# Kernel tuning notes

Measured on AMD Instinct MI355X. Metric: run time of the kernel, lower is better.

The kernel has to match this reference:

```python
import jax, jax.numpy as jnp
import numpy as np

NUM_CENTROIDS = 64
NUM_KMEANS = 5
KM_ITERS = 20


def _kmeans_labels(X, key):
    """Lloyd k-means on X [N,D]; returns final cluster labels [N] (int32).
    Mirrors faiss.Kmeans(dim, num_centroids, niter=...) label assignment."""
    N, D = X.shape
    idx = jax.random.choice(key, N, (NUM_CENTROIDS,), replace=False)
    cent0 = X[idx]  # [C,D] init from random data points

    def assign(cent):
        d = (cent * cent).sum(-1)[None, :] - 2.0 * (X @ cent.T)  # [N,C]
        return jnp.argmin(d, axis=1)

    def step(cent, _):
        lab = assign(cent)
        sums = jax.ops.segment_sum(X, lab, num_segments=NUM_CENTROIDS)  # [C,D]
        cnts = jax.ops.segment_sum(jnp.ones((N,), X.dtype), lab, num_segments=NUM_CENTROIDS)
        newc = jnp.where(cnts[:, None] > 0, sums / jnp.maximum(cnts, 1.0)[:, None], cent)
        return newc, None

    cent, _ = jax.lax.scan(step, cent0, None, length=KM_ITERS)
    return assign(cent)


def setup_inputs() -> dict:
    key = jax.random.key(0)
    k1, k2, k3 = jax.random.split(key, 3)
    N, D = 8192, 512
    adj = jax.random.uniform(k1, (N, N), dtype=jnp.float32)
    student = jax.random.normal(k2, (N, D), dtype=jnp.float32)
    teacher = jax.random.normal(k3, (N, D), dtype=jnp.float32)
    return {"adj": adj, "student": student, "teacher": teacher, "topk": 16}


def reference(adj, student, teacher, topk):
    N, D = student.shape
    # similarity = (student @ teacher.T).detach() + 10*I
    sim = jax.lax.stop_gradient(student @ teacher.T) + 10.0 * jnp.eye(N, dtype=student.dtype)
    _, I_knn = jax.lax.top_k(sim, topk)  # [N, k], sorted descending
    rows = jnp.arange(N)[:, None]  # [N,1]

    # knn_neighbor: sparse ones at (row, I_knn); topk cols are distinct per row
    knn_pat = jnp.zeros((N, N), adj.dtype).at[rows, I_knn].set(1.0)
    locality = knn_pat * adj  # sparse elementwise product knn_neighbor * adj

    # k-means cluster labels over NUM_KMEANS seeds (teacher is detached/cpu in torch)
    Xt = jax.lax.stop_gradient(teacher)
    keys = jax.random.split(jax.random.key(1234), NUM_KMEANS)
    labels = jax.vmap(lambda k: _kmeans_labels(Xt, k))(keys)  # [M,N]

    # close-in-background mask: any seed where label(i) == label(knn_j(i))
    ngh_lab = labels[:, I_knn]               # [M,N,k]
    mask = jnp.any(labels[:, :, None] == ngh_lab, axis=0)  # [N,k]

    # globality: ones at masked (row, knn) positions
    glob_pat = jnp.zeros((N, N), adj.dtype).at[rows, I_knn].add(mask.astype(adj.dtype))

    # pos = locality + globality (dense equivalent of coalesced sparse sum)
    pos = locality + glob_pat
    return pos
```

## Files before the change

kernel.cpp:

```cpp
#include <hip/hip_runtime.h>
#include <stdint.h>

typedef unsigned int u32;
typedef unsigned long long u64;
typedef __attribute__((ext_vector_type(8))) short short8;
typedef __attribute__((ext_vector_type(4))) float f32x4;

#define NN 8192
#define DD 512
#define CC 64
#define RR 5
#define KM_ITERS 20
#define TOPKK 16
#define CHUNK 4096
#define GAP_TH 0.05f
#define FLAGTH 0.02f
#define BAND_TH 0.01f
#define FIXCAP (RR * NN)
#define TK_LO 256.0f
#define TK_SCALE 8.0f

#define MFMA_BF16 __builtin_amdgcn_mfma_f32_16x16x32_bf16

__device__ __forceinline__ void gload16(void* lds, const void* g) {
  __builtin_amdgcn_global_load_lds(
      (const __attribute__((address_space(1))) void*)g,
      (__attribute__((address_space(3))) void*)lds, 16, 0, 0);
}

__device__ __forceinline__ u32 keyenc(float v) {
  u32 u = __float_as_uint(v);
  return (u & 0x80000000u) ? ~u : (u | 0x80000000u);
}
__device__ __forceinline__ int tkbin(float v) {
  int b = (int)((v + TK_LO) * TK_SCALE);
  return b < 0 ? 0 : (b > 4095 ? 4095 : b);
}

__device__ __forceinline__ void tf2x32(u32 k0, u32 k1, u32 x0, u32 x1,
                                       u32& o0, u32& o1) {
  u32 ks2 = k0 ^ k1 ^ 0x1BD11BDAu;
  x0 += k0; x1 += k1;
#define TFR(r) { x0 += x1; x1 = (x1 << r) | (x1 >> (32 - r)); x1 ^= x0; }
  TFR(13) TFR(15) TFR(26) TFR(6)
  x0 += k1; x1 += ks2 + 1u;
  TFR(17) TFR(29) TFR(16) TFR(24)
  x0 += ks2; x1 += k0 + 2u;
  TFR(13) TFR(15) TFR(26) TFR(6)
  x0 += k0; x1 += k1 + 3u;
  TFR(17) TFR(29) TFR(16) TFR(24)
  x0 += k1; x1 += ks2 + 4u;
  TFR(13) TFR(15) TFR(26) TFR(6)
  x0 += ks2; x1 += k0 + 5u;
#undef TFR
  o0 = x0; o1 = x1;
}

__global__ __launch_bounds__(256) void rng_kernel(u32* __restrict__ bits1,
                                                  u32* __restrict__ bits2) {
  int r = blockIdx.x;
  int i = blockIdx.y * 256 + threadIdx.x;
  u32 rk0, rk1; tf2x32(0u, 1234u, 0u, (u32)r, rk0, rk1);
  u32 k10, k11, s10, s11, s20, s21;
  tf2x32(rk0, rk1, 0u, 0u, k10, k11);
  tf2x32(rk0, rk1, 0u, 1u, s10, s11);
  tf2x32(k10, k11, 0u, 1u, s20, s21);
  u32 a, b;
  tf2x32(s10, s11, 0u, (u32)i, a, b);
  bits1[r * NN + i] = a ^ b;
  tf2x32(s20, s21, 0u, (u32)i, a, b);
  bits2[r * NN + i] = a ^ b;
}

__global__ __launch_bounds__(256) void rankpart_kernel(const u32* __restrict__ bits,
                                                       u32* __restrict__ prank) {
  __shared__ u64 sk[2048];
  int r = blockIdx.x, zc = blockIdx.z;
  const u32* bb = bits + (size_t)r * NN;
  int jbase = zc * 2048;
  for (int t = threadIdx.x; t < 2048; t += 256)
    sk[t] = ((u64)bb[jbase + t] << 13) | (u32)(jbase + t);
  __syncthreads();
  int i = blockIdx.y * 256 + threadIdx.x;
  u64 ki = ((u64)bb[i] << 13) | (u32)i;
  int cnt = 0;
#pragma unroll 8
  for (int j = 0; j < 2048; ++j) cnt += (int)(sk[j] < ki);
  prank[(size_t)(r * 4 + zc) * NN + i] = cnt;
}

__global__ __launch_bounds__(256) void scat1_kernel(const u32* __restrict__ prank,
                                                    int* __restrict__ vout) {
  int r = blockIdx.x;
  int i = blockIdx.y * 256 + threadIdx.x;
  int rank = prank[(size_t)(r * 4 + 0) * NN + i] + prank[(size_t)(r * 4 + 1) * NN + i] +
             prank[(size_t)(r * 4 + 2) * NN + i] + prank[(size_t)(r * 4 + 3) * NN + i];
  vout[(size_t)r * NN + rank] = i;
}

__global__ __launch_bounds__(256) void scat2_kernel(const u32* __restrict__ prank,
                                                    const int* __restrict__ v1,
                                                    int* __restrict__ sel) {
  int r = blockIdx.x;
  int i = blockIdx.y * 256 + threadIdx.x;
  int rank = prank[(size_t)(r * 4 + 0) * NN + i] + prank[(size_t)(r * 4 + 1) * NN + i] +
             prank[(size_t)(r * 4 + 2) * NN + i] + prank[(size_t)(r * 4 + 3) * NN + i];
  if (rank < CC) sel[r * CC + rank] = v1[(size_t)r * NN + i];
}

__device__ __forceinline__ double block_reduce_d(double s, double* red4) {
  int tid = threadIdx.x;
  for (int off = 32; off > 0; off >>= 1) s += __shfl_down(s, off, 64);
  if ((tid & 63) == 0) red4[tid >> 6] = s;
  __syncthreads();
  return red4[0] + red4[1] + red4[2] + red4[3];
}

__device__ __forceinline__ u32 bf16rne(float a) {
  u32 ab = __float_as_uint(a);
  return (ab + 0x7FFFu + ((ab >> 16) & 1u)) >> 16;
}
__device__ __forceinline__ void splitf(float a, unsigned short& hi, unsigned short& lo) {
  u32 h = bf16rne(a);
  float hf = __uint_as_float(h << 16);
  hi = (unsigned short)h;
  lo = (unsigned short)bf16rne(a - hf);
}

__global__ __launch_bounds__(256) void init_cent_kernel(const float* __restrict__ X,
                                                        const int* __restrict__ sel,
                                                        double* __restrict__ centD,
                                                        double* __restrict__ cnD,
                                                        float* __restrict__ cnF,
                                                        unsigned short* __restrict__ CHg,
                                                        unsigned short* __restrict__ CLg) {
  __shared__ double red4[4];
  int r = blockIdx.x, c = blockIdx.y, t = threadIdx.x;
  int src = sel[r * CC + c];
  const float* xp = X + (size_t)src * DD;
  size_t o = (size_t)(r * CC + c) * DD;
  double va = (double)xp[t], vb = (double)xp[t + 256];
  centD[o + t] = va; centD[o + t + 256] = vb;
  unsigned short h0, l0, h1, l1;
  splitf((float)va, h0, l0); splitf((float)vb, h1, l1);
  CHg[o + t] = h0; CLg[o + t] = l0;
  CHg[o + t + 256] = h1; CLg[o + t + 256] = l1;
  double tot = block_reduce_d(va * va + vb * vb, red4);
  if (t == 0) { cnD[r * CC + c] = tot; cnF[r * CC + c] = (float)tot; }
}

__global__ __launch_bounds__(256) void split_kernel(const float* __restrict__ in,
                                                    unsigned short* __restrict__ hi,
                                                    unsigned short* __restrict__ lo) {
  size_t base = ((size_t)blockIdx.x * 256 + threadIdx.x) * 8;
  float4 v0 = *(const float4*)(in + base);
  float4 v1 = *(const float4*)(in + base + 4);
  float vv[8] = {v0.x, v0.y, v0.z, v0.w, v1.x, v1.y, v1.z, v1.w};
  unsigned short h[8], l[8];
#pragma unroll
  for (int j = 0; j < 8; ++j) splitf(vv[j], h[j], l[j]);
  uint4 hv, lv;
  hv.x = h[0] | ((u32)h[1] << 16); hv.y = h[2] | ((u32)h[3] << 16);
  hv.z = h[4] | ((u32)h[5] << 16); hv.w = h[6] | ((u32)h[7] << 16);
  lv.x = l[0] | ((u32)l[1] << 16); lv.y = l[2] | ((u32)l[3] << 16);
  lv.z = l[4] | ((u32)l[5] << 16); lv.w = l[6] | ((u32)l[7] << 16);
  *(uint4*)(hi + base) = hv;
  *(uint4*)(lo + base) = lv;
}

__global__ __launch_bounds__(256) void assign_kernel(const unsigned short* __restrict__ XH,
                                                     const unsigned short* __restrict__ XL,
                                                     const unsigned short* __restrict__ CHg,
                                                     const unsigned short* __restrict__ CLg,
                                                     const float* __restrict__ cnF,
                                                     int* __restrict__ labels,
                                                     u32* __restrict__ flags,
                                                     u32* __restrict__ counter) {
  __shared__ unsigned short Xh[2 * 64 * 32], Xl[2 * 64 * 32],
                            Ch[2 * 64 * 32], Cl[2 * 64 * 32];
  __shared__ float dmat[64 * 68];
  int r = blockIdx.y;
  int blk = blockIdx.x;
  int rowBase = blk * 64;
  int tid = threadIdx.x;
  int wid = tid >> 6, lane = tid & 63, m = lane & 15, q = lane >> 4;
  int srow = wid * 16 + (lane >> 2);
  int sslot = (lane & 3) * 8;
  const unsigned short* gxh = XH + (size_t)(rowBase + srow) * DD + sslot;
  const unsigned short* gxl = XL + (size_t)(rowBase + srow) * DD + sslot;
  const unsigned short* gch = CHg + ((size_t)r * CC + srow) * DD + sslot;
  const unsigned short* gcl = CLg + ((size_t)r * CC + srow) * DD + sslot;
  f32x4 acc[4] = {};
  for (int kc = 0; kc < DD; kc += 64) {
#pragma unroll
    for (int p = 0; p < 2; ++p) {
      int off = p * 2048, ko = kc + p * 32;
      gload16(&Xh[off + wid * 512], gxh + ko);
      gload16(&Xl[off + wid * 512], gxl + ko);
      gload16(&Ch[off + wid * 512], gch + ko);
      gload16(&Cl[off + wid * 512], gcl + ko);
    }
    __syncthreads();
#pragma unroll
    for (int s = 0; s < 2; ++s) {
      int off = s * 2048;
      short8 ah = *(short8*)&Xh[off + (wid * 16 + m) * 32 + q * 8];
      short8 al = *(short8*)&Xl[off + (wid * 16 + m) * 32 + q * 8];
#pragma unroll
      for (int nt = 0; nt < 4; ++nt) {
        short8 bh = *(short8*)&Ch[off + (nt * 16 + m) * 32 + q * 8];
        short8 bl = *(short8*)&Cl[off + (nt * 16 + m) * 32 + q * 8];
        acc[nt] = MFMA_BF16(ah, bh, acc[nt], 0, 0, 0);
        acc[nt] = MFMA_BF16(ah, bl, acc[nt], 0, 0, 0);
        acc[nt] = MFMA_BF16(al, bh, acc[nt], 0, 0, 0);
      }
    }
    __syncthreads();
  }
#pragma unroll
  for (int nt = 0; nt < 4; ++nt) {
    float cn = cnF[r * CC + nt * 16 + m];
#pragma unroll
    for (int reg = 0; reg < 4; ++reg)
      dmat[(wid * 16 + q * 4 + reg) * 68 + nt * 16 + m] = cn - 2.0f * acc[nt][reg];
  }
  __syncthreads();
  if (tid < 64) {
    const float* dr = dmat + (size_t)tid * 68;
    float best = dr[0], second = 3.4e38f; int bi = 0;
    for (int c = 1; c < CC; ++c) {
      float v = dr[c];
      if (v < best) { second = best; best = v; bi = c; }
      else if (v < second) second = v;
    }
    labels[(size_t)r * NN + rowBase + tid] = bi;
    if (second - best < GAP_TH) {
      u32 idx = atomicAdd(counter, 1u);
      if (idx < FIXCAP) flags[idx] = (u32)(r * NN + rowBase + tid);
    }
  }
}

__global__ __launch_bounds__(256) void fixup_kernel(const float* __restrict__ X,
                                                    const double* __restrict__ centD,
                                                    const double* __restrict__ cnD,
                                                    const u32* __restrict__ flags,
                                                    const u32* __restrict__ counter,
                                                    int* __restrict__ labels) {
  __shared__ double darr[CC];
  int n = (int)*counter; if (n > FIXCAP) n = FIXCAP;
  int tid = threadIdx.x, c = tid >> 2, sub = tid & 3;
  for (int f = blockIdx.x; f < n; f += gridDim.x) {
    u32 pk = flags[f];
    int r = pk >> 13, i = pk & (NN - 1);
    const float* x = X + (size_t)i * DD + sub * 128;
    const double* cp = centD + (size_t)(r * CC + c) * DD + sub * 128;
    double s = 0.0;
    for (int k = 0; k < 128; ++k) s += (double)x[k] * cp[k];
    s += __shfl_down(s, 2, 64);
    s += __shfl_down(s, 1, 64);
    if (sub == 0) darr[c] = cnD[r * CC + c] - 2.0 * s;
    __syncthreads();
    if (tid == 0) {
      double best = darr[0]; int bi = 0;
      for (int cc = 1; cc < CC; ++cc) { double v = darr[cc]; if (v < best) { best = v; bi = cc; } }
      labels[(size_t)r * NN + i] = bi;
    }
    __syncthreads();
  }
}

__global__ __launch_bounds__(64) void hist_kernel(const int* __restrict__ labels,
                                                  int* __restrict__ bhist,
                                                  int* __restrict__ rib) {
  __shared__ int labs[64];
  __shared__ int h[CC];
  int r = blockIdx.y, blk = blockIdx.x, tid = threadIdx.x;
  labs[tid] = labels[(size_t)r * NN + blk * 64 + tid];
  h[tid] = 0;
  __syncthreads();
  int lab = labs[tid];
  atomicAdd(&h[lab], 1);
  int rk = 0;
  for (int j = 0; j < tid; ++j) rk += (labs[j] == lab);
  rib[(size_t)r * NN + blk * 64 + tid] = rk;
  __syncthreads();
  bhist[(size_t)(r * 128 + blk) * CC + tid] = h[tid];
}

__global__ __launch_bounds__(256) void fill_kernel(const int* __restrict__ labels,
                                                   const int* __restrict__ rib,
                                                   const int* __restrict__ bhist,
                                                   int* __restrict__ cstart,
                                                   int* __restrict__ cnt,
                                                   int* __restrict__ member) {
  __shared__ int bh[128 * CC];
  __shared__ int cs[CC];
  __shared__ int tots[CC];
  int r = blockIdx.x, blk = blockIdx.y, tid = threadIdx.x;
  const int* src = bhist + (size_t)r * 128 * CC;
  for (int t = tid; t < 128 * CC; t += 256) bh[t] = src[t];
  __syncthreads();
  if (tid < CC) {
    int run = 0;
    for (int b = 0; b < 128; ++b) { int v = bh[b * CC + tid]; bh[b * CC + tid] = run; run += v; }
    tots[tid] = run;
  }
  __syncthreads();
  if (tid == 0) {
    int run = 0;
    for (int q2 = 0; q2 < CC; ++q2) { cs[q2] = run; run += tots[q2]; }
  }
  __syncthreads();
  int i = blk * 256 + tid;
  int lab = labels[(size_t)r * NN + i];
  int pos = cs[lab] + bh[(i >> 6) * CC + lab] + rib[(size_t)r * NN + i];
  member[(size_t)r * NN + pos] = i;
  if (blk == 0 && tid < CC) { cnt[r * CC + tid] = tots[tid]; cstart[r * CC + tid] = cs[tid]; }
}

__global__ __launch_bounds__(256) void update_kernel(const float* __restrict__ X,
                                                     const int* __restrict__ member,
                                                     const int* __restrict__ cstart,
                                                     const int* __restrict__ cnt,
                                                     const double* __restrict__ centOld,
                                                     double* __restrict__ centNew) {
  __shared__ double part[4][64];
  int r = blockIdx.x, c = blockIdx.y, dchunk = blockIdx.z;
  int tid = threadIdx.x;
  int d = dchunk * 64 + (tid & 63);
  int lane = tid >> 6;
  int n = cnt[r * CC + c];
  int st = cstart[r * CC + c];
  const int* mem = member + (size_t)r * NN + st;
  int n4 = (n + 3) >> 2;
  int lo = lane * n4;
  int hi = min(n, lo + n4);
  double s0 = 0, s1 = 0, s2 = 0, s3 = 0;
  int m = lo;
  for (; m + 3 < hi; m += 4) {
    s0 += (double)X[(size_t)mem[m + 0] * DD + d];
    s1 += (double)X[(size_t)mem[m + 1] * DD + d];
    s2 += (double)X[(size_t)mem[m + 2] * DD + d];
    s3 += (double)X[(size_t)mem[m + 3] * DD + d];
  }
  for (; m < hi; ++m) s0 += (double)X[(size_t)mem[m] * DD + d];
  part[lane][tid & 63] = (s0 + s1) + (s2 + s3);
  __syncthreads();
  if (tid < 64) {
    double tot = (part[0][tid] + part[1][tid]) + (part[2][tid] + part[3][tid]);
    size_t o = (size_t)(r * CC + c) * DD + dchunk * 64 + tid;
    double va = (n > 0) ? tot / (double)n : centOld[o];
    centNew[o] = va;
  }
}

__global__ __launch_bounds__(256) void norm_kernel(const double* __restrict__ centNew,
                                                   double* __restrict__ cnD,
                                                   float* __restrict__ cnF,
                                                   unsigned short* __restrict__ CHg,
                                                   unsigned short* __restrict__ CLg) {
  __shared__ double red4[4];
  int r = blockIdx.x, c = blockIdx.y, t = threadIdx.x;
  size_t o = (size_t)(r * CC + c) * DD;
  double va = centNew[o + t], vb = centNew[o + t + 256];
  unsigned short h0, l0, h1, l1;
  splitf((float)va, h0, l0); splitf((float)vb, h1, l1);
  CHg[o + t] = h0; CLg[o + t] = l0;
  CHg[o + t + 256] = h1; CLg[o + t + 256] = l1;
  double tot = block_reduce_d(va * va + vb * vb, red4);
  if (t == 0) { cnD[r * CC + c] = tot; cnF[r * CC + c] = (float)tot; }
}

__global__ __launch_bounds__(256) void gemm_kernel(const unsigned short* __restrict__ SH,
                                                   const unsigned short* __restrict__ SL,
                                                   const unsigned short* __restrict__ TH,
                                                   const unsigned short* __restrict__ TL,
                                                   float* __restrict__ sim,
                                                   int rowChunk) {
  __shared__ unsigned short Ah[2 * 128 * 32], Al[2 * 128 * 32],
                            Bh[2 * 128 * 32], Bl[2 * 128 * 32];
  int tid = threadIdx.x;
  int wid = tid >> 6, lane = tid & 63, m = lane & 15, q = lane >> 4;
  int waveM = wid >> 1, waveN = wid & 1;
  const int nwgx = NN / 128;
  const int nwg = nwgx * (CHUNK / 128);
  int wg = blockIdx.y * nwgx + blockIdx.x;
  int swz = (wg & 7) * (nwg >> 3) + (wg >> 3);
  int rowTile = swz / nwgx, colTile = swz % nwgx;
  int rowBase = rowChunk + rowTile * 128;
  int colBase = colTile * 128;
  int sr0 = wid * 16 + (lane >> 2);
  int sr1 = (wid + 4) * 16 + (lane >> 2);
  int sslot = (lane & 3) * 8;
  const unsigned short* gah0 = SH + (size_t)(rowBase + sr0) * DD + sslot;
  const unsigned short* gah1 = SH + (size_t)(rowBase + sr1) * DD + sslot;
  const unsigned short* gal0 = SL + (size_t)(rowBase + sr0) * DD + sslot;
  const unsigned short* gal1 = SL + (size_t)(rowBase + sr1) * DD + sslot;
  const unsigned short* gbh0 = TH + (size_t)(colBase + sr0) * DD + sslot;
  const unsigned short* gbh1 = TH + (size_t)(colBase + sr1) * DD + sslot;
  const unsigned short* gbl0 = TL + (size_t)(colBase + sr0) * DD + sslot;
  const unsigned short* gbl1 = TL + (size_t)(colBase + sr1) * DD + sslot;
  f32x4 acc[4][4] = {};
  for (int kc = 0; kc < DD; kc += 64) {
#pragma unroll
    for (int p = 0; p < 2; ++p) {
      int off = p * 4096, ko = kc + p * 32;
      gload16(&Ah[off + wid * 512], gah0 + ko);
      gload16(&Ah[off + (wid + 4) * 512], gah1 + ko);
      gload16(&Al[off + wid * 512], gal0 + ko);
      gload16(&Al[off + (wid + 4) * 512], gal1 + ko);
      gload16(&Bh[off + wid * 512], gbh0 + ko);
      gload16(&Bh[off + (wid + 4) * 512], gbh1 + ko);
      gload16(&Bl[off + wid * 512], gbl0 + ko);
      gload16(&Bl[off + (wid + 4) * 512], gbl1 + ko);
    }
    __syncthreads();
#pragma unroll
    for (int s = 0; s < 2; ++s) {
      int off = s * 4096;
      short8 ah[4], al[4], bh[4], bl[4];
#pragma unroll
      for (int t = 0; t < 4; ++t) {
        ah[t] = *(short8*)&Ah[off + (waveM * 64 + t * 16 + m) * 32 + q * 8];
        al[t] = *(short8*)&Al[off + (waveM * 64 + t * 16 + m) * 32 + q * 8];
        bh[t] = *(short8*)&Bh[off + (waveN * 64 + t * 16 + m) * 32 + q * 8];
        bl[t] = *(short8*)&Bl[off + (waveN * 64 + t * 16 + m) * 32 + q * 8];
      }
#pragma unroll
      for (int mt = 0; mt < 4; ++mt)
#pragma unroll
        for (int nt = 0; nt < 4; ++nt) {
          acc[mt][nt] = MFMA_BF16(ah[mt], bh[nt], acc[mt][nt], 0, 0, 0);
          acc[mt][nt] = MFMA_BF16(ah[mt], bl[nt], acc[mt][nt], 0, 0, 0);
          acc[mt][nt] = MFMA_BF16(al[mt], bh[nt], acc[mt][nt], 0, 0, 0);
        }
    }
    __syncthreads();
  }
#pragma unroll
  for (int mt = 0; mt < 4; ++mt)
#pragma unroll
    for (int nt = 0; nt < 4; ++nt) {
      int gcol = colBase + waveN * 64 + nt * 16 + m;
#pragma unroll
      for (int reg = 0; reg < 4; ++reg) {
        int lrow = rowTile * 128 + waveM * 64 + mt * 16 + q * 4 + reg;
        int grow = rowChunk + lrow;
        float v = acc[mt][nt][reg];
        if (grow == gcol) v += 10.0f;
        sim[(size_t)lrow * NN + gcol] = v;
      }
    }
}

__global__ __launch_bounds__(256) void topk_kernel(const float* __restrict__ sim,
                                                   const float* __restrict__ S,
                                                   const float* __restrict__ T,
                                                   int* __restrict__ iknn,
                                                   int rowChunk) {
  __shared__ int bins[4096];
  __shared__ int partial[256];
  __shared__ u64 cand[128];
  __shared__ u64 sure[24];
  __shared__ u64 outk[TOPKK + 1];
  __shared__ u64 red[4];
  __shared__ int nsure, ncand, selB1, hardcase;
  __shared__ int nsureR, nbandR;
  __shared__ int sidx[16];
  __shared__ int bidx[64];
  __shared__ double bval[64];

  int blk = blockIdx.x, tid = threadIdx.x;
  int grow = rowChunk + blk;
  const float* rp = sim + (size_t)blk * NN;

  for (int t = tid; t < 4096; t += 256) bins[t] = 0;
  if (tid == 0) { nsure = 0; ncand = 0; hardcase = 0; }
  __syncthreads();
  for (int t = tid; t < NN; t += 256) atomicAdd(&bins[tkbin(rp[t])], 1);
  __syncthreads();
  int ps = 0;
#pragma unroll
  for (int b = 0; b < 16; ++b) ps += bins[tid * 16 + b];
  partial[tid] = ps;
  __syncthreads();
  if (tid == 0) {
    int cum = 0, c = 255;
    for (; c > 0; --c) { if (cum + partial[c] >= 17) break; cum += partial[c]; }
    int b = c * 16 + 15;
    for (; b > c * 16; --b) { if (cum + bins[b] >= 17) break; cum += bins[b]; }
    selB1 = b;
  }
  __syncthreads();
  int B1 = selB1;
  for (int t = tid; t < NN; t += 256) {
    float v = rp[t];
    int b = tkbin(v);
    if (b < B1) continue;
    u64 key = ((u64)keyenc(v) << 32) | (u32)(NN - 1 - t);
    if (b > B1) { int s = atomicAdd(&nsure, 1); if (s < 24) sure[s] = key; }
    else        { int s = atomicAdd(&ncand, 1); if (s < 128) cand[s] = key; }
  }
  __syncthreads();
  if (tid == 0 && ncand > 128) hardcase = 1;
  __syncthreads();
  if (!hardcase) {
    int ns = nsure, nc = ncand;
    int total = ns + nc;
    if (tid < total) {
      u64 k = tid < ns ? sure[tid] : cand[tid - ns];
      int rank = 0;
      for (int j = 0; j < total; ++j) {
        u64 o = j < ns ? sure[j] : cand[j - ns];
        rank += (int)(o > k);
      }
      if (rank < TOPKK + 1) outk[rank] = k;
    }
    __syncthreads();
  } else {
    for (int k = 0; k < TOPKK + 1; ++k) {
      u64 best = 0;
      for (int t = tid; t < NN; t += 256) {
        u64 key = ((u64)keyenc(rp[t]) << 32) | (u32)(NN - 1 - t);
        bool excl = false;
        for (int j = 0; j < k; ++j) excl |= (outk[j] == key);
        if (!excl && key > best) best = key;
      }
      for (int off = 32; off > 0; off >>= 1) {
        u32 lo = (u32)best, hi = (u32)(best >> 32);
        lo = __shfl_down(lo, off, 64); hi = __shfl_down(hi, off, 64);
        u64 o = ((u64)hi << 32) | lo;
        best = o > best ? o : best;
      }
      if ((tid & 63) == 0) red[tid >> 6] = best;
      __syncthreads();
      if (tid == 0) {
        u64 b = red[0];
        for (int w = 1; w < 4; ++w) b = red[w] > b ? red[w] : b;
        outk[k] = b;
      }
      __syncthreads();
    }
  }
  if (tid < TOPKK)
    iknn[(size_t)grow * TOPKK + tid] = (NN - 1) - (int)(outk[tid] & 0xFFFFFFFFu);
  u32 ub16 = (u32)(outk[TOPKK - 1] >> 32), ub17 = (u32)(outk[TOPKK] >> 32);
  float v16 = (ub16 & 0x80000000u) ? __uint_as_float(ub16 & 0x7FFFFFFFu)
                                   : __uint_as_float(~ub16);
  float v17 = (ub17 & 0x80000000u) ? __uint_as_float(ub17 & 0x7FFFFFFFu)
                                   : __uint_as_float(~ub17);
  if (v16 - v17 >= FLAGTH) return;

  if (tid == 0) { nsureR = 0; nbandR = 0; }
  __syncthreads();
  for (int j = tid; j < NN; j += 256) {
    float v = rp[j];
    if (v > v16 + BAND_TH) {
      int s = atomicAdd(&nsureR, 1);
      if (s < 16) sidx[s] = j;
    } else if (v >= v16 - BAND_TH) {
      int s = atomicAdd(&nbandR, 1);
      if (s < 64) bidx[s] = j;
    }
  }
  __syncthreads();
  int nb = nbandR > 64 ? 64 : nbandR;
  if (tid < nb) {
    const float* sp = S + (size_t)grow * DD;
    const float* tp = T + (size_t)bidx[tid] * DD;
    double s = 0.0;
    for (int k = 0; k < DD; ++k) s += (double)sp[k] * (double)tp[k];
    bval[tid] = s;
  }
  __syncthreads();
  if (tid == 0) {
    int w = 0;
    int ns = nsureR < 16 ? nsureR : 16;
    for (int i2 = 0; i2 < ns; ++i2) iknn[(size_t)grow * TOPKK + w++] = sidx[i2];
    u64 used = 0;
    while (w < TOPKK) {
      int bj = -1; double bv = 0.0;
      for (int i2 = 0; i2 < nb; ++i2) {
        if (used & (1ull << i2)) continue;
        if (bj < 0 || bval[i2] > bv ||
            (bval[i2] == bv && bidx[i2] < bidx[bj])) { bv = bval[i2]; bj = i2; }
      }
      if (bj < 0) break;
      used |= 1ull << bj;
      iknn[(size_t)grow * TOPKK + w++] = bidx[bj];
    }
  }
}

__global__ __launch_bounds__(256) void zero_kernel(float4* __restrict__ out) {
  size_t i = (size_t)blockIdx.x * 256 + threadIdx.x;
  out[i] = make_float4(0.f, 0.f, 0.f, 0.f);
}

__global__ void zeroc_kernel(u32* __restrict__ c) {
  c[threadIdx.x] = 0u;
}

__global__ __launch_bounds__(256) void scatter_kernel(const float* __restrict__ adj,
                                                      const int* __restrict__ iknn,
                                                      const int* __restrict__ labels,
                                                      float* __restrict__ out) {
  int idx = blockIdx.x * 256 + threadIdx.x;
  int i = idx >> 4;
  int col = iknn[idx];
  int m = 0;
#pragma unroll
  for (int r = 0; r < RR; ++r)
    m |= (labels[(size_t)r * NN + i] == labels[(size_t)r * NN + col]);
  size_t o = (size_t)i * NN + col;
  out[o] = adj[o] + (float)m;
}

extern "C" void kernel_launch(void* const* d_in, const int* in_sizes, int n_in,
                              void* d_out, int out_size, void* d_ws, size_t ws_size,
                              hipStream_t stream) {
  (void)in_sizes; (void)n_in; (void)out_size; (void)ws_size;
  const float* adj     = (const float*)d_in[0];
  const float* student = (const float*)d_in[1];
  const float* teacher = (const float*)d_in[2];
  float* out = (float*)d_out;

  char* p = (char*)d_ws;
  auto alloc = [&](size_t bytes) -> void* {
    void* q = (void*)p; p += (bytes + 255) & ~(size_t)255; return q;
  };
  double* centA  = (double*)alloc((size_t)RR * CC * DD * 8);
  double* centB  = (double*)alloc((size_t)RR * CC * DD * 8);
  double* cnD    = (double*)alloc((size_t)RR * CC * 8);
  float*  cnF    = (float*) alloc((size_t)RR * CC * 4);
  u32*    bits1  = (u32*)   alloc((size_t)RR * NN * 4);
  u32*    bits2  = (u32*)   alloc((size_t)RR * NN * 4);
  u32*    prank  = (u32*)   alloc((size_t)RR * 4 * NN * 4);
  int*    v1     = (int*)   alloc((size_t)RR * NN * 4);
  int*    sel    = (int*)   alloc((size_t)RR * CC * 4);
  int*    labels = (int*)   alloc((size_t)RR * NN * 4);
  int*    bhist  = (int*)   alloc((size_t)RR * 128 * CC * 4);
  int*    cstart = (int*)   alloc((size_t)RR * CC * 4);
  int*    cnt    = (int*)   alloc((size_t)RR * CC * 4);
  int*    rib    = (int*)   alloc((size_t)RR * NN * 4);
  int*    member = (int*)   alloc((size_t)RR * NN * 4);
  u32*    flags  = (u32*)   alloc((size_t)FIXCAP * 4);
  u32*    counters = (u32*) alloc((size_t)64 * 4);
  int*    iknn   = (int*)   alloc((size_t)NN * TOPKK * 4);
  unsigned short* SH = (unsigned short*)alloc((size_t)NN * DD * 2);
  unsigned short* SL = (unsigned short*)alloc((size_t)NN * DD * 2);
  unsigned short* THi = (unsigned short*)alloc((size_t)NN * DD * 2);
  unsigned short* TLo = (unsigned short*)alloc((size_t)NN * DD * 2);
  unsigned short* CHg = (unsigned short*)alloc((size_t)RR * CC * DD * 2);
  unsigned short* CLg = (unsigned short*)alloc((size_t)RR * CC * DD * 2);
  float*  simc   = (float*) alloc((size_t)CHUNK * NN * 4);

  zeroc_kernel<<<1, 64, 0, stream>>>(counters);

  rng_kernel<<<dim3(RR, 32), 256, 0, stream>>>(bits1, bits2);
  rankpart_kernel<<<dim3(RR, 32, 4), 256, 0, stream>>>(bits1, prank);
  scat1_kernel<<<dim3(RR, 32), 256, 0, stream>>>(prank, v1);
  rankpart_kernel<<<dim3(RR, 32, 4), 256, 0, stream>>>(bits2, prank);
  scat2_kernel<<<dim3(RR, 32), 256, 0, stream>>>(prank, v1, sel);
  init_cent_kernel<<<dim3(RR, CC), 256, 0, stream>>>(teacher, sel, centA, cnD, cnF, CHg, CLg);

  split_kernel<<<(NN * DD / 8) / 256, 256, 0, stream>>>(student, SH, SL);
  split_kernel<<<(NN * DD / 8) / 256, 256, 0, stream>>>(teacher, THi, TLo);

  double* cur = centA; double* nxt = centB;
  for (int it = 0; it < KM_ITERS; ++it) {
    assign_kernel<<<dim3(NN / 64, RR), 256, 0, stream>>>(THi, TLo, CHg, CLg, cnF,
                                                         labels, flags, counters + it);
    fixup_kernel<<<2048, 256, 0, stream>>>(teacher, cur, cnD, flags, counters + it, labels);
    hist_kernel<<<dim3(128, RR), 64, 0, stream>>>(labels, bhist, rib);
    fill_kernel<<<dim3(RR, 32), 256, 0, stream>>>(labels, rib, bhist, cstart, cnt, member);
    update_kernel<<<dim3(RR, CC, 8), 256, 0, stream>>>(teacher, member, cstart, cnt, cur, nxt);
    norm_kernel<<<dim3(RR, CC), 256, 0, stream>>>(nxt, cnD, cnF, CHg, CLg);
    double* t = cur; cur = nxt; nxt = t;
  }
  assign_kernel<<<dim3(NN / 64, RR), 256, 0, stream>>>(THi, TLo, CHg, CLg, cnF,
                                                       labels, flags, counters + KM_ITERS);
  fixup_kernel<<<2048, 256, 0, stream>>>(teacher, cur, cnD, flags,
                                         counters + KM_ITERS, labels);

  for (int ch = 0; ch < NN / CHUNK; ++ch) {
    gemm_kernel<<<dim3(NN / 128, CHUNK / 128), 256, 0, stream>>>(SH, SL, THi, TLo, simc,
                                                                 ch * CHUNK);
    topk_kernel<<<CHUNK, 256, 0, stream>>>(simc, student, teacher, iknn, ch * CHUNK);
  }

  zero_kernel<<<(unsigned)((size_t)NN * NN / 4 / 256), 256, 0, stream>>>((float4*)out);
  scatter_kernel<<<NN * TOPKK / 256, 256, 0, stream>>>(adj, iknn, labels, out);
}
```

Measured before the change: 2.601 ms.

## Fuse histogram into fill and centroid norm/split into update kernel

Removes hist_kernel by having each fill block load all labels into LDS and build the per-group histograms and in-group ranks itself. Removes norm_kernel by letting update_kernel write the hi/lo bf16 split and accumulate the centroid squared norm via a wave reduction plus a double atomicAdd. The float copy of the norms is dropped and assign reads the double norms directly. This cuts two launches and intermediate buffers per k-means iteration. The cost is redundant histogram work across fill blocks and nondeterministic atomic summation order for the norms.

```diff
diff --git a/kernel.cpp b/kernel.cpp
--- a/kernel.cpp
+++ b/kernel.cpp
@@ -131,7 +131,6 @@
                                                         const int* __restrict__ sel,
                                                         double* __restrict__ centD,
                                                         double* __restrict__ cnD,
-                                                        float* __restrict__ cnF,
                                                         unsigned short* __restrict__ CHg,
                                                         unsigned short* __restrict__ CLg) {
   __shared__ double red4[4];
@@ -146,7 +145,7 @@
   CHg[o + t] = h0; CLg[o + t] = l0;
   CHg[o + t + 256] = h1; CLg[o + t + 256] = l1;
   double tot = block_reduce_d(va * va + vb * vb, red4);
-  if (t == 0) { cnD[r * CC + c] = tot; cnF[r * CC + c] = (float)tot; }
+  if (t == 0) cnD[r * CC + c] = tot;
 }
 
 __global__ __launch_bounds__(256) void split_kernel(const float* __restrict__ in,
@@ -172,7 +171,7 @@
                                                      const unsigned short* __restrict__ XL,
                                                      const unsigned short* __restrict__ CHg,
                                                      const unsigned short* __restrict__ CLg,
-                                                     const float* __restrict__ cnF,
+                                                     const double* __restrict__ cnDin,
                                                      int* __restrict__ labels,
                                                      u32* __restrict__ flags,
                                                      u32* __restrict__ counter) {
@@ -219,7 +218,7 @@
   }
 #pragma unroll
   for (int nt = 0; nt < 4; ++nt) {
-    float cn = cnF[r * CC + nt * 16 + m];
+    float cn = (float)cnDin[r * CC + nt * 16 + m];
 #pragma unroll
     for (int reg = 0; reg < 4; ++reg)
       dmat[(wid * 16 + q * 4 + reg) * 68 + nt * 16 + m] = cn - 2.0f * acc[nt][reg];
@@ -270,40 +269,30 @@
   }
 }
 
-__global__ __launch_bounds__(64) void hist_kernel(const int* __restrict__ labels,
-                                                  int* __restrict__ bhist,
-                                                  int* __restrict__ rib) {
-  __shared__ int labs[64];
-  __shared__ int h[CC];
-  int r = blockIdx.y, blk = blockIdx.x, tid = threadIdx.x;
-  labs[tid] = labels[(size_t)r * NN + blk * 64 + tid];
-  h[tid] = 0;
-  __syncthreads();
-  int lab = labs[tid];
-  atomicAdd(&h[lab], 1);
-  int rk = 0;
-  for (int j = 0; j < tid; ++j) rk += (labs[j] == lab);
-  rib[(size_t)r * NN + blk * 64 + tid] = rk;
-  __syncthreads();
-  bhist[(size_t)(r * 128 + blk) * CC + tid] = h[tid];
-}
-
 __global__ __launch_bounds__(256) void fill_kernel(const int* __restrict__ labels,
-                                                   const int* __restrict__ rib,
-                                                   const int* __restrict__ bhist,
                                                    int* __restrict__ cstart,
                                                    int* __restrict__ cnt,
-                                                   int* __restrict__ member) {
-  __shared__ int bh[128 * CC];
+                                                   int* __restrict__ member,
+                                                   double* __restrict__ cnD) {
+  __shared__ int labsS[NN];
+  __shared__ int bh[128 * 65];
   __shared__ int cs[CC];
   __shared__ int tots[CC];
   int r = blockIdx.x, blk = blockIdx.y, tid = threadIdx.x;
-  const int* src = bhist + (size_t)r * 128 * CC;
-  for (int t = tid; t < 128 * CC; t += 256) bh[t] = src[t];
+  const int* lr = labels + (size_t)r * NN;
+  for (int t = tid; t < NN; t += 256) labsS[t] = lr[t];
+  for (int t = tid; t < 128 * 65; t += 256) bh[t] = 0;
+  __syncthreads();
+  if (tid < 128) {
+    int g = tid;
+    int* hrow = &bh[g * 65];
+    const int* ls = &labsS[g * 64];
+    for (int j = 0; j < 64; ++j) ++hrow[ls[j]];
+  }
   __syncthreads();
   if (tid < CC) {
     int run = 0;
-    for (int b = 0; b < 128; ++b) { int v = bh[b * CC + tid]; bh[b * CC + tid] = run; run += v; }
+    for (int b = 0; b < 128; ++b) { int v = bh[b * 65 + tid]; bh[b * 65 + tid] = run; run += v; }
     tots[tid] = run;
   }
   __syncthreads();
@@ -313,10 +302,17 @@
   }
   __syncthreads();
   int i = blk * 256 + tid;
-  int lab = labels[(size_t)r * NN + i];
-  int pos = cs[lab] + bh[(i >> 6) * CC + lab] + rib[(size_t)r * NN + i];
+  int lab = labsS[i];
+  int g = i >> 6;
+  int rk = 0;
+  for (int j = g * 64; j < i; ++j) rk += (labsS[j] == lab);
+  int pos = cs[lab] + bh[g * 65 + lab] + rk;
   member[(size_t)r * NN + pos] = i;
-  if (blk == 0 && tid < CC) { cnt[r * CC + tid] = tots[tid]; cstart[r * CC + tid] = cs[tid]; }
+  if (blk == 0 && tid < CC) {
+    cnt[r * CC + tid] = tots[tid];
+    cstart[r * CC + tid] = cs[tid];
+    cnD[r * CC + tid] = 0.0;
+  }
 }
 
 __global__ __launch_bounds__(256) void update_kernel(const float* __restrict__ X,
@@ -324,7 +320,10 @@
                                                      const int* __restrict__ cstart,
                                                      const int* __restrict__ cnt,
                                                      const double* __restrict__ centOld,
-                                                     double* __restrict__ centNew) {
+                                                     double* __restrict__ centNew,
+                                                     double* __restrict__ cnD,
+                                                     unsigned short* __restrict__ CHg,
+                                                     unsigned short* __restrict__ CLg) {
   __shared__ double part[4][64];
   int r = blockIdx.x, c = blockIdx.y, dchunk = blockIdx.z;
   int tid = threadIdx.x;
@@ -352,24 +351,13 @@
     size_t o = (size_t)(r * CC + c) * DD + dchunk * 64 + tid;
     double va = (n > 0) ? tot / (double)n : centOld[o];
     centNew[o] = va;
-  }
-}
-
-__global__ __launch_bounds__(256) void norm_kernel(const double* __restrict__ centNew,
-                                                   double* __restrict__ cnD,
-                                                   float* __restrict__ cnF,
-                                                   unsigned short* __restrict__ CHg,
-                                                   unsigned short* __restrict__ CLg) {
-  __shared__ double red4[4];
-  int r = blockIdx.x, c = blockIdx.y, t = threadIdx.x;
-  size_t o = (size_t)(r * CC + c) * DD;
-  double va = centNew[o + t], vb = centNew[o + t + 256];
-  unsigned short h0, l0, h1, l1;
-  splitf((float)va, h0, l0); splitf((float)vb, h1, l1);
-  CHg[o + t] = h0; CLg[o + t] = l0;
-  CHg[o + t + 256] = h1; CLg[o + t + 256] = l1;
-  double tot = block_reduce_d(va * va + vb * vb, red4);
-  if (t == 0) { cnD[r * CC + c] = tot; cnF[r * CC + c] = (float)tot; }
+    unsigned short h0, l0;
+    splitf((float)va, h0, l0);
+    CHg[o] = h0; CLg[o] = l0;
+    double nsum = va * va;
+    for (int off = 32; off > 0; off >>= 1) nsum += __shfl_down(nsum, off, 64);
+    if (tid == 0) atomicAdd(&cnD[r * CC + c], nsum);
+  }
 }
 
 __global__ __launch_bounds__(256) void gemm_kernel(const unsigned short* __restrict__ SH,
@@ -633,17 +621,14 @@
   double* centA  = (double*)alloc((size_t)RR * CC * DD * 8);
   double* centB  = (double*)alloc((size_t)RR * CC * DD * 8);
   double* cnD    = (double*)alloc((size_t)RR * CC * 8);
-  float*  cnF    = (float*) alloc((size_t)RR * CC * 4);
   u32*    bits1  = (u32*)   alloc((size_t)RR * NN * 4);
   u32*    bits2  = (u32*)   alloc((size_t)RR * NN * 4);
   u32*    prank  = (u32*)   alloc((size_t)RR * 4 * NN * 4);
   int*    v1     = (int*)   alloc((size_t)RR * NN * 4);
   int*    sel    = (int*)   alloc((size_t)RR * CC * 4);
   int*    labels = (int*)   alloc((size_t)RR * NN * 4);
-  int*    bhist  = (int*)   alloc((size_t)RR * 128 * CC * 4);
   int*    cstart = (int*)   alloc((size_t)RR * CC * 4);
   int*    cnt    = (int*)   alloc((size_t)RR * CC * 4);
-  int*    rib    = (int*)   alloc((size_t)RR * NN * 4);
   int*    member = (int*)   alloc((size_t)RR * NN * 4);
   u32*    flags  = (u32*)   alloc((size_t)FIXCAP * 4);
   u32*    counters = (u32*) alloc((size_t)64 * 4);
@@ -663,23 +648,22 @@
   scat1_kernel<<<dim3(RR, 32), 256, 0, stream>>>(prank, v1);
   rankpart_kernel<<<dim3(RR, 32, 4), 256, 0, stream>>>(bits2, prank);
   scat2_kernel<<<dim3(RR, 32), 256, 0, stream>>>(prank, v1, sel);
-  init_cent_kernel<<<dim3(RR, CC), 256, 0, stream>>>(teacher, sel, centA, cnD, cnF, CHg, CLg);
+  init_cent_kernel<<<dim3(RR, CC), 256, 0, stream>>>(teacher, sel, centA, cnD, CHg, CLg);
 
   split_kernel<<<(NN * DD / 8) / 256, 256, 0, stream>>>(student, SH, SL);
   split_kernel<<<(NN * DD / 8) / 256, 256, 0, stream>>>(teacher, THi, TLo);
 
   double* cur = centA; double* nxt = centB;
   for (int it = 0; it < KM_ITERS; ++it) {
-    assign_kernel<<<dim3(NN / 64, RR), 256, 0, stream>>>(THi, TLo, CHg, CLg, cnF,
+    assign_kernel<<<dim3(NN / 64, RR), 256, 0, stream>>>(THi, TLo, CHg, CLg, cnD,
                                                          labels, flags, counters + it);
     fixup_kernel<<<2048, 256, 0, stream>>>(teacher, cur, cnD, flags, counters + it, labels);
-    hist_kernel<<<dim3(128, RR), 64, 0, stream>>>(labels, bhist, rib);
-    fill_kernel<<<dim3(RR, 32), 256, 0, stream>>>(labels, rib, bhist, cstart, cnt, member);
-    update_kernel<<<dim3(RR, CC, 8), 256, 0, stream>>>(teacher, member, cstart, cnt, cur, nxt);
-    norm_kernel<<<dim3(RR, CC), 256, 0, stream>>>(nxt, cnD, cnF, CHg, CLg);
+    fill_kernel<<<dim3(RR, 32), 256, 0, stream>>>(labels, cstart, cnt, member, cnD);
+    update_kernel<<<dim3(RR, CC, 8), 256, 0, stream>>>(teacher, member, cstart, cnt,
+                                                       cur, nxt, cnD, CHg, CLg);
     double* t = cur; cur = nxt; nxt = t;
   }
-  assign_kernel<<<dim3(NN / 64, RR), 256, 0, stream>>>(THi, TLo, CHg, CLg, cnF,
+  assign_kernel<<<dim3(NN / 64, RR), 256, 0, stream>>>(THi, TLo, CHg, CLg, cnD,
                                                        labels, flags, counters + KM_ITERS);
   fixup_kernel<<<2048, 256, 0, stream>>>(teacher, cur, cnD, flags,
                                          counters + KM_ITERS, labels);
```

Result: no change. 2.624 ms (+0.9%).

## Replace sort-based centroid update with LDS atomic accumulation per cluster

Applied to the files above, without the earlier changes.

The hist/fill/update pipeline, which builds per-cluster member lists before gathering rows, is replaced by a single accumulation kernel. Each block adds its rows into a shared-memory per-cluster double accumulator with atomics, then flushes the non-zero partials to global sums with atomics. A finalize kernel divides by the counts, computes norms and does the bf16 split. This removes two launches and the scattered gather per iteration, at the cost of float64 atomic contention and summation order that is no longer deterministic, which could in principle flip labels that sit near a tie.

```diff
diff --git a/kernel.cpp b/kernel.cpp
--- a/kernel.cpp
+++ b/kernel.cpp
@@ -270,100 +270,59 @@
   }
 }
 
-__global__ __launch_bounds__(64) void hist_kernel(const int* __restrict__ labels,
-                                                  int* __restrict__ bhist,
-                                                  int* __restrict__ rib) {
-  __shared__ int labs[64];
-  __shared__ int h[CC];
-  int r = blockIdx.y, blk = blockIdx.x, tid = threadIdx.x;
-  labs[tid] = labels[(size_t)r * NN + blk * 64 + tid];
-  h[tid] = 0;
-  __syncthreads();
-  int lab = labs[tid];
-  atomicAdd(&h[lab], 1);
-  int rk = 0;
-  for (int j = 0; j < tid; ++j) rk += (labs[j] == lab);
-  rib[(size_t)r * NN + blk * 64 + tid] = rk;
-  __syncthreads();
-  bhist[(size_t)(r * 128 + blk) * CC + tid] = h[tid];
-}
-
-__global__ __launch_bounds__(256) void fill_kernel(const int* __restrict__ labels,
-                                                   const int* __restrict__ rib,
-                                                   const int* __restrict__ bhist,
-                                                   int* __restrict__ cstart,
-                                                   int* __restrict__ cnt,
-                                                   int* __restrict__ member) {
-  __shared__ int bh[128 * CC];
-  __shared__ int cs[CC];
-  __shared__ int tots[CC];
-  int r = blockIdx.x, blk = blockIdx.y, tid = threadIdx.x;
-  const int* src = bhist + (size_t)r * 128 * CC;
-  for (int t = tid; t < 128 * CC; t += 256) bh[t] = src[t];
-  __syncthreads();
-  if (tid < CC) {
-    int run = 0;
-    for (int b = 0; b < 128; ++b) { int v = bh[b * CC + tid]; bh[b * CC + tid] = run; run += v; }
-    tots[tid] = run;
-  }
-  __syncthreads();
-  if (tid == 0) {
-    int run = 0;
-    for (int q2 = 0; q2 < CC; ++q2) { cs[q2] = run; run += tots[q2]; }
-  }
-  __syncthreads();
-  int i = blk * 256 + tid;
-  int lab = labels[(size_t)r * NN + i];
-  int pos = cs[lab] + bh[(i >> 6) * CC + lab] + rib[(size_t)r * NN + i];
-  member[(size_t)r * NN + pos] = i;
-  if (blk == 0 && tid < CC) { cnt[r * CC + tid] = tots[tid]; cstart[r * CC + tid] = cs[tid]; }
-}
-
-__global__ __launch_bounds__(256) void update_kernel(const float* __restrict__ X,
-                                                     const int* __restrict__ member,
-                                                     const int* __restrict__ cstart,
-                                                     const int* __restrict__ cnt,
-                                                     const double* __restrict__ centOld,
-                                                     double* __restrict__ centNew) {
-  __shared__ double part[4][64];
-  int r = blockIdx.x, c = blockIdx.y, dchunk = blockIdx.z;
-  int tid = threadIdx.x;
-  int d = dchunk * 64 + (tid & 63);
-  int lane = tid >> 6;
-  int n = cnt[r * CC + c];
-  int st = cstart[r * CC + c];
-  const int* mem = member + (size_t)r * NN + st;
-  int n4 = (n + 3) >> 2;
-  int lo = lane * n4;
-  int hi = min(n, lo + n4);
-  double s0 = 0, s1 = 0, s2 = 0, s3 = 0;
-  int m = lo;
-  for (; m + 3 < hi; m += 4) {
-    s0 += (double)X[(size_t)mem[m + 0] * DD + d];
-    s1 += (double)X[(size_t)mem[m + 1] * DD + d];
-    s2 += (double)X[(size_t)mem[m + 2] * DD + d];
-    s3 += (double)X[(size_t)mem[m + 3] * DD + d];
-  }
-  for (; m < hi; ++m) s0 += (double)X[(size_t)mem[m] * DD + d];
-  part[lane][tid & 63] = (s0 + s1) + (s2 + s3);
-  __syncthreads();
-  if (tid < 64) {
-    double tot = (part[0][tid] + part[1][tid]) + (part[2][tid] + part[3][tid]);
-    size_t o = (size_t)(r * CC + c) * DD + dchunk * 64 + tid;
-    double va = (n > 0) ? tot / (double)n : centOld[o];
-    centNew[o] = va;
-  }
-}
-
-__global__ __launch_bounds__(256) void norm_kernel(const double* __restrict__ centNew,
-                                                   double* __restrict__ cnD,
-                                                   float* __restrict__ cnF,
-                                                   unsigned short* __restrict__ CHg,
-                                                   unsigned short* __restrict__ CLg) {
+__global__ __launch_bounds__(256) void zerosum_kernel(double* __restrict__ centSum,
+                                                      int* __restrict__ cnt) {
+  int flat = blockIdx.x * 256 + threadIdx.x;
+  centSum[flat] = 0.0;
+  if (flat < RR * CC) cnt[flat] = 0;
+}
+
+__global__ __launch_bounds__(256) void accum_kernel(const float* __restrict__ X,
+                                                    const int* __restrict__ labels,
+                                                    double* __restrict__ centSum,
+                                                    int* __restrict__ cnt) {
+  __shared__ double lacc[CC * 64];
+  __shared__ int lcnt[CC];
+  int r = blockIdx.x, rb = blockIdx.y, dc = blockIdx.z;
+  int tid = threadIdx.x, w = tid >> 6, lane = tid & 63;
+  for (int t = tid; t < CC * 64; t += 256) lacc[t] = 0.0;
+  if (tid < CC) lcnt[tid] = 0;
+  __syncthreads();
+  const int* lab = labels + (size_t)r * NN + rb * 256 + w * 64;
+  const float* xp = X + (size_t)(rb * 256 + w * 64) * DD + dc * 64 + lane;
+#pragma unroll 4
+  for (int j = 0; j < 64; ++j) {
+    int c = lab[j];
+    float x = xp[(size_t)j * DD];
+    atomicAdd(&lacc[c * 64 + lane], (double)x);
+    if (dc == 0 && lane == 0) atomicAdd(&lcnt[c], 1);
+  }
+  __syncthreads();
+  for (int t = tid; t < CC * 64; t += 256) {
+    double v = lacc[t];
+    if (v != 0.0) {
+      int c = t >> 6, dim = t & 63;
+      unsafeAtomicAdd(&centSum[((size_t)r * CC + c) * DD + dc * 64 + dim], v);
+    }
+  }
+  if (dc == 0 && tid < CC && lcnt[tid] > 0) atomicAdd(&cnt[r * CC + tid], lcnt[tid]);
+}
+
+__global__ __launch_bounds__(256) void finalize_kernel(const double* __restrict__ centSum,
+                                                       const int* __restrict__ cnt,
+                                                       const double* __restrict__ centOld,
+                                                       double* __restrict__ centNew,
+                                                       double* __restrict__ cnD,
+                                                       float* __restrict__ cnF,
+                                                       unsigned short* __restrict__ CHg,
+                                                       unsigned short* __restrict__ CLg) {
   __shared__ double red4[4];
   int r = blockIdx.x, c = blockIdx.y, t = threadIdx.x;
   size_t o = (size_t)(r * CC + c) * DD;
-  double va = centNew[o + t], vb = centNew[o + t + 256];
+  int n = cnt[r * CC + c];
+  double va = (n > 0) ? centSum[o + t] / (double)n : centOld[o + t];
+  double vb = (n > 0) ? centSum[o + t + 256] / (double)n : centOld[o + t + 256];
+  centNew[o + t] = va; centNew[o + t + 256] = vb;
   unsigned short h0, l0, h1, l1;
   splitf((float)va, h0, l0); splitf((float)vb, h1, l1);
   CHg[o + t] = h0; CLg[o + t] = l0;
@@ -632,6 +591,7 @@
   };
   double* centA  = (double*)alloc((size_t)RR * CC * DD * 8);
   double* centB  = (double*)alloc((size_t)RR * CC * DD * 8);
+  double* centSum= (double*)alloc((size_t)RR * CC * DD * 8);
   double* cnD    = (double*)alloc((size_t)RR * CC * 8);
   float*  cnF    = (float*) alloc((size_t)RR * CC * 4);
   u32*    bits1  = (u32*)   alloc((size_t)RR * NN * 4);
@@ -640,11 +600,7 @@
   int*    v1     = (int*)   alloc((size_t)RR * NN * 4);
   int*    sel    = (int*)   alloc((size_t)RR * CC * 4);
   int*    labels = (int*)   alloc((size_t)RR * NN * 4);
-  int*    bhist  = (int*)   alloc((size_t)RR * 128 * CC * 4);
-  int*    cstart = (int*)   alloc((size_t)RR * CC * 4);
   int*    cnt    = (int*)   alloc((size_t)RR * CC * 4);
-  int*    rib    = (int*)   alloc((size_t)RR * NN * 4);
-  int*    member = (int*)   alloc((size_t)RR * NN * 4);
   u32*    flags  = (u32*)   alloc((size_t)FIXCAP * 4);
   u32*    counters = (u32*) alloc((size_t)64 * 4);
   int*    iknn   = (int*)   alloc((size_t)NN * TOPKK * 4);
@@ -672,11 +628,12 @@
   for (int it = 0; it < KM_ITERS; ++it) {
     assign_kernel<<<dim3(NN / 64, RR), 256, 0, stream>>>(THi, TLo, CHg, CLg, cnF,
                                                          labels, flags, counters + it);
+    zerosum_kernel<<<640, 256, 0, stream>>>(centSum, cnt);
     fixup_kernel<<<2048, 256, 0, stream>>>(teacher, cur, cnD, flags, counters + it, labels);
-    hist_kernel<<<dim3(128, RR), 64, 0, stream>>>(labels, bhist, rib);
-    fill_kernel<<<dim3(RR, 32), 256, 0, stream>>>(labels, rib, bhist, cstart, cnt, member);
-    update_kernel<<<dim3(RR, CC, 8), 256, 0, stream>>>(teacher, member, cstart, cnt, cur, nxt);
-    norm_kernel<<<dim3(RR, CC), 256, 0, stream>>>(nxt, cnD, cnF, CHg, CLg);
+    accum_kernel<<<dim3(RR, NN / 256, DD / 64), 256, 0, stream>>>(teacher, labels,
+                                                                  centSum, cnt);
+    finalize_kernel<<<dim3(RR, CC), 256, 0, stream>>>(centSum, cnt, cur, nxt,
+                                                      cnD, cnF, CHg, CLg);
     double* t = cur; cur = nxt; nxt = t;
   }
   assign_kernel<<<dim3(NN / 64, RR), 256, 0, stream>>>(THi, TLo, CHg, CLg, cnF,
```

After: 2.873 ms. 1.1x slower.
